# Performance work log

Measured on AMD Instinct MI355X. Metric: run time of the kernel, lower is better.

Reference implementation:

```python
import jax, jax.numpy as jnp
import numpy as np

K = 3
KK = K * K


def conv3x3(x, w, b):
    # x: [B,C,H,W], w: [O,C,3,3]
    y = jax.lax.conv_general_dilated(x, w, (1, 1), ((1, 1), (1, 1)),
                                     dimension_numbers=('NCHW', 'OIHW', 'NCHW'))
    return y + b[None, :, None, None]


def deform_conv(x, offset, w, b):
    # torchvision.ops.deform_conv2d, 3x3, pad=1, stride=1, no mask.
    B, C, H, W = x.shape
    off = offset.reshape(B, KK, 2, H, W)  # per kernel tap: (dy, dx)
    ky = jnp.repeat(jnp.arange(K, dtype=x.dtype) - 1, K)  # [9]
    kx = jnp.tile(jnp.arange(K, dtype=x.dtype) - 1, K)
    py = jnp.arange(H, dtype=x.dtype)[None, None, :, None] + ky[None, :, None, None] + off[:, :, 0]
    px = jnp.arange(W, dtype=x.dtype)[None, None, None, :] + kx[None, :, None, None] + off[:, :, 1]
    y0 = jnp.floor(py)
    x0 = jnp.floor(px)
    wy = (py - y0)[:, None]  # [B,1,9,H,W]
    wx = (px - x0)[:, None]
    y0i = y0.astype(jnp.int32)
    x0i = x0.astype(jnp.int32)
    xf = x.reshape(B, C, H * W)

    def corner(yi, xi):
        valid = ((yi >= 0) & (yi < H) & (xi >= 0) & (xi < W))
        idx = jnp.clip(yi, 0, H - 1) * W + jnp.clip(xi, 0, W - 1)  # [B,9,H,W]
        g = jax.vmap(lambda xb, ib: xb[:, ib.reshape(-1)])(xf, idx)  # [B,C,9*H*W]
        return g.reshape(B, C, KK, H, W) * valid[:, None].astype(x.dtype)

    val = (corner(y0i, x0i) * (1 - wy) * (1 - wx)
           + corner(y0i, x0i + 1) * (1 - wy) * wx
           + corner(y0i + 1, x0i) * wy * (1 - wx)
           + corner(y0i + 1, x0i + 1) * wy * wx)  # [B,C,9,H,W]
    out = jnp.einsum('bckhw,ock->bohw', val, w.reshape(w.shape[0], C, KK))
    return out + b[None, :, None, None]


def se_gate(x, w1, b1, w2, b2):
    # global avg pool -> 1x1 conv -> relu -> 1x1 conv -> sigmoid -> scale
    m = x.mean((2, 3))  # [B,C]
    h = jax.nn.relu(jnp.einsum('bc,rc->br', m, w1) + b1)
    g = jax.nn.sigmoid(jnp.einsum('br,cr->bc', h, w2) + b2)
    return x * g[:, :, None, None]


def resize_bilinear(x, oh, ow):
    # F.interpolate(mode='bilinear', align_corners=False)
    B, C, H, W = x.shape

    def coords(n_in, n_out):
        src = (jnp.arange(n_out, dtype=x.dtype) + 0.5) * (n_in / n_out) - 0.5
        src = jnp.clip(src, 0.0, n_in - 1)
        i0 = jnp.floor(src).astype(jnp.int32)
        i1 = jnp.minimum(i0 + 1, n_in - 1)
        return i0, i1, (src - i0).astype(x.dtype)

    y0, y1, wy = coords(H, oh)
    x = x[:, :, y0, :] * (1 - wy)[None, None, :, None] + x[:, :, y1, :] * wy[None, None, :, None]
    c0, c1, wc = coords(W, ow)
    x = x[:, :, :, c0] * (1 - wc)[None, None, None, :] + x[:, :, :, c1] * wc[None, None, None, :]
    return x


def setup_inputs() -> dict:
    key = jax.random.key(0)
    ks = jax.random.split(key, 12)
    B, C, H, W = 4, 64, 128, 128
    L, O, R = 4, 64, 4  # levels, out_channels, reduction=64//16
    d = {
        'x': jax.random.normal(ks[0], (B, C, H, W), jnp.float32),
        'off_w': jax.random.normal(ks[1], (L, 2 * KK, C, 3, 3), jnp.float32) * 0.01,
        'off_b': jax.random.normal(ks[2], (L, 2 * KK), jnp.float32) * 0.01,
        'dc_w': jax.random.normal(ks[3], (L, O, C, 3, 3), jnp.float32) * 0.05,
        'dc_b': jax.random.normal(ks[4], (L, O), jnp.float32) * 0.05,
        'se_w1': jax.random.normal(ks[5], (L, R, O), jnp.float32) * 0.1,
        'se_b1': jax.random.normal(ks[6], (L, R), jnp.float32) * 0.1,
        'se_w2': jax.random.normal(ks[7], (L, O, R), jnp.float32) * 0.1,
        'se_b2': jax.random.normal(ks[8], (L, O), jnp.float32) * 0.1,
        'fuse_w': jax.random.normal(ks[9], (O, L * O), jnp.float32) * 0.05,
        'fuse_b': jax.random.normal(ks[10], (O,), jnp.float32) * 0.05,
    }
    return d


def reference(x, off_w, off_b, dc_w, dc_b, se_w1, se_b1, se_w2, se_b2, fuse_w, fuse_b):
    B, _, H, W = x.shape
    L = off_w.shape[0]
    cur = x
    feats = []
    for i in range(L):
        if i > 0:
            cur = resize_bilinear(cur, cur.shape[2] // 2, cur.shape[3] // 2)
        off = conv3x3(cur, off_w[i], off_b[i])
        cur = deform_conv(cur, off, dc_w[i], dc_b[i])
        cur = se_gate(cur, se_w1[i], se_b1[i], se_w2[i], se_b2[i])
        feats.append(resize_bilinear(cur, H, W))
    for i in range(L - 2, -1, -1):
        feats[i] = feats[i] + feats[i + 1]
    fused = jnp.concatenate(feats, axis=1)  # [B, L*O, H, W]
    return jnp.einsum('bchw,oc->bohw', fused, fuse_w) + fuse_b[None, :, None, None]
```

## Files before the change

### kernel.cpp

```cpp
#include <hip/hip_runtime.h>
#include <hip/hip_bf16.h>
#include <math.h>


constexpr int Bn = 4;

typedef __attribute__((ext_vector_type(8))) short short8;
typedef __attribute__((ext_vector_type(4))) float f32x4;
typedef __attribute__((ext_vector_type(4))) unsigned uint4v;
typedef __attribute__((ext_vector_type(4))) unsigned short ushort4v;

static __device__ __forceinline__ short f2b(float f){
  union { float f; unsigned u; } v; v.f = f;
  unsigned r = v.u + 0x7fffu + ((v.u >> 16) & 1u);
  return (short)(r >> 16);
}
static __device__ __forceinline__ unsigned f2b2(float x, float y){
  union { __hip_bfloat162 h; unsigned u; } cv;
  cv.h = __float22bfloat162_rn(make_float2(x, y));
  return cv.u;
}
static __device__ __forceinline__ float blo(unsigned u){ return __uint_as_float(u << 16); }
static __device__ __forceinline__ float bhi(unsigned u){ return __uint_as_float(u & 0xffff0000u); }
static __device__ __forceinline__ void pinv(uint4v& x){ asm volatile("" : "+v"(x)); }

constexpr size_t OFF_CUR   = 0;
constexpr size_t OFF_DC    = OFF_CUR  + 4194304;
constexpr size_t OFF_T0    = OFF_DC   + 4194304;
constexpr size_t OFF_T1    = OFF_T0   + 4194304;
constexpr size_t OFF_T2    = OFF_T1   + 1048576;
constexpr size_t OFF_T3    = OFF_T2   + 262144;
constexpr size_t OFF_WSUMT = OFF_T3   + 65536;
constexpr size_t OFF_DCWT  = OFF_WSUMT + 8192;
constexpr size_t OFF_OWT   = OFF_DCWT  + 73728;
constexpr size_t OFF_SUMS  = OFF_OWT   + 36864;

__global__ void prep_k(const float* __restrict__ dc_w, const float* __restrict__ off_w,
                       const float* __restrict__ fuse_w, float* __restrict__ ws){
  int i = blockIdx.x * 256 + threadIdx.x;
  short* dcwT  = (short*)(ws + OFF_DCWT);
  short* owT   = (short*)(ws + OFF_OWT);
  short* wsumT = (short*)(ws + OFF_WSUMT);
  if (i < 147456){
    int oc = i / 576, r = i % 576, k = r >> 6, c = r & 63;
    dcwT[i] = f2b(dc_w[(oc*64 + c)*9 + k]);
  } else if (i < 147456 + 73728){
    int t = i - 147456;
    int lm = t / 576, l = lm >> 5, m = lm & 31, r = t % 576, k = r >> 6, c = r & 63;
    owT[t] = (m < 18) ? f2b(off_w[((l*18 + m)*64 + c)*9 + k]) : (short)0;
  } else if (i < 147456 + 73728 + 16384){
    int t = i - (147456 + 73728);
    int l = t / 4096, r = t % 4096, o = r / 64, c = r % 64;
    float s = 0.f;
    for (int jl = 0; jl <= l; jl++) s += fuse_w[o*256 + jl*64 + c];
    wsumT[t] = f2b(s);
  } else if (i < 147456 + 73728 + 16384 + 65536){
    ws[OFF_SUMS + (i - (147456 + 73728 + 16384))] = 0.f;
  }
}

__global__ __launch_bounds__(256) void cvt_k(const float* __restrict__ x, unsigned* __restrict__ cur){
  __shared__ float t[64][65];
  int tile = blockIdx.x;
  int b = tile >> 8, p0 = (tile & 255) << 6;
  int tx = threadIdx.x & 63, ty = threadIdx.x >> 6;
  #pragma unroll
  for (int c = ty; c < 64; c += 4)
    t[c][tx] = x[(((size_t)(b << 6) + c) << 14) + p0 + tx];
  __syncthreads();
  int u = threadIdx.x & 31, pr = threadIdx.x >> 5;
  #pragma unroll
  for (int i = 0; i < 8; i++){
    int pp = pr + i*8;
    unsigned v = f2b2(t[2*u][pp], t[2*u + 1][pp]);
    cur[((size_t)(b << 14) + p0 + pp)*32 + u] = v;
  }
}

template<int H, int LVL>
__global__ __launch_bounds__(256, 3) void deform8_k(
    const unsigned* __restrict__ cur, const float* __restrict__ ws_all,
    const float* __restrict__ off_bias, const float* __restrict__ dc_bias,
    float* __restrict__ dc, float* __restrict__ sums){
  constexpr int W = H, P = H * W;
  constexpr int PITCHB = 584 * 2;
  constexpr int TPR8 = W/8, TPB8 = P/64;
  __shared__ __align__(16) short valA[16][584];
  __shared__ __align__(16) char  patchS[64*144];
  __shared__ __align__(16) float4 tapW[144];
  __shared__ __align__(8)  unsigned short tapIs[144][4];
  float* offsP = (float*)((char*)&valA[0][0] + 8192);
  const short* owt = (const short*)(ws_all + OFF_OWT) + LVL * 32 * 576;
  const short* dcw = (const short*)(ws_all + OFF_DCWT) + (size_t)LVL * 64 * 576;
  const int tid = threadIdx.x;
  const int wave = tid >> 6, lane = tid & 63;
  const int c0 = lane & 15, quad = lane >> 4, q4 = quad * 4;
  const int b = blockIdx.x / TPB8;
  const int rr = blockIdx.x % TPB8;
  const int hrow8 = (rr / TPR8) * 8, wcol8 = (rr % TPR8) * 8;
  const unsigned* curu = cur + (size_t)b * P * 32;

  uint4v wB[9];
  {
    const short* wrow = owt + ((wave & 1)*16 + c0)*576 + quad*8;
    #pragma unroll
    for (int kb = 0; kb < 9; kb++)
      wB[kb] = *(const uint4v*)&wrow[((wave >> 1)*9 + kb)*32];
    #pragma unroll
    for (int kb = 0; kb < 9; kb++) pinv(wB[kb]);
  }
  const int n = wave*16 + c0;
  uint4v wD[18];
  #pragma unroll
  for (int kb = 0; kb < 18; kb++)
    wD[kb] = *(const uint4v*)&dcw[n*576 + kb*32 + quad*8];
  #pragma unroll
  for (int kb = 0; kb < 18; kb++) pinv(wD[kb]);
  const float bt2 = dc_bias[LVL*64 + n];
  const int tk = tid % 9, tp = tid / 9;
  float oby = 0.f, obx = 0.f;
  if (tid < 144){
    oby = off_bias[LVL*18 + 2*tk];
    obx = off_bias[LVL*18 + 2*tk + 1];
  }
  const int pl = lane >> 3, cq = lane & 7;

  #pragma unroll 1
  for (int t = 0; t < 4; t++){
    const int srow = hrow8 + (t >> 1)*4, scol = wcol8 + (t & 1)*4;
    if (t) __syncthreads();

    #pragma unroll
    for (int i = 0; i < 2; i++){
      int pp = wave*16 + i*8 + pl;
      int R = pp >> 3, C = pp & 7;
      int yy = srow - 2 + R, xx = scol - 2 + C;
      bool v = ((unsigned)yy < (unsigned)H) & ((unsigned)xx < (unsigned)W);
      int idx = v ? (yy*W + xx) : 0;
      uint4 d = *(const uint4*)((const char*)curu + (size_t)idx*128 + cq*16);
      if (!v){ d.x = 0; d.y = 0; d.z = 0; d.w = 0; }
      *(uint4*)(patchS + pp*144 + cq*16) = d;
    }
    __syncthreads();

    {
      const int colw = wave & 1, kh = wave >> 1;
      const char* pb = patchS + (((c0 >> 2) + 1)*8 + (c0 & 3) + 1)*144 + quad*16;
      f32x4 oacc = {0,0,0,0};
      if (kh == 0){
        #pragma unroll
        for (int kb = 0; kb < 9; kb++){
          const int tap = kb >> 1;
          short8 a = *(const short8*)(pb + ((tap/3)*8 + (tap%3))*144 + (kb&1)*64);
          oacc = __builtin_amdgcn_mfma_f32_16x16x32_bf16(a, __builtin_bit_cast(short8, wB[kb]), oacc, 0, 0, 0);
        }
      } else {
        #pragma unroll
        for (int kb = 0; kb < 9; kb++){
          const int kk = 9 + kb, tap = kk >> 1;
          short8 a = *(const short8*)(pb + ((tap/3)*8 + (tap%3))*144 + (kk&1)*64);
          oacc = __builtin_amdgcn_mfma_f32_16x16x32_bf16(a, __builtin_bit_cast(short8, wB[kb]), oacc, 0, 0, 0);
        }
      }
      int comp = colw*16 + c0;
      if (comp < 18){
        #pragma unroll
        for (int r = 0; r < 4; r++) offsP[kh*288 + (q4 + r)*18 + comp] = oacc[r];
      }
    }
    __syncthreads();

    if (tid < 144){
      int p = tp, k = tk;
      int h = srow + (p >> 2), w = scol + (p & 3);
      float oy = offsP[p*18 + 2*k]     + offsP[288 + p*18 + 2*k]     + oby;
      float ox = offsP[p*18 + 2*k + 1] + offsP[288 + p*18 + 2*k + 1] + obx;
      float py = (float)(h + k/3 - 1) + oy;
      float px = (float)(w + k%3 - 1) + ox;
      float y0f = floorf(py), x0f = floorf(px);
      float fy = py - y0f, fx = px - x0f;
      int y0 = (int)y0f, x0 = (int)x0f, y1 = y0 + 1, x1 = x0 + 1;
      bool vy0 = (y0 >= 0) & (y0 < H), vy1 = (y1 >= 0) & (y1 < H);
      bool vx0 = (x0 >= 0) & (x0 < W), vx1 = (x1 >= 0) & (x1 < W);
      int y0c = min(max(y0, 0), H-1), y1c = min(max(y1, 0), H-1);
      int x0c = min(max(x0, 0), W-1), x1c = min(max(x1, 0), W-1);
      float gy = 1.f - fy, gx = 1.f - fx;
      tapW[tid] = make_float4((vy0 & vx0) ? gy*gx : 0.f,
                              (vy0 & vx1) ? gy*fx : 0.f,
                              (vy1 & vx0) ? fy*gx : 0.f,
                              (vy1 & vx1) ? fy*fx : 0.f);
      int ry = y0 - srow + 2, rx = x0 - scol + 2;
      if (((unsigned)ry < 7u) & ((unsigned)rx < 7u)){
        tapIs[tid][0] = (unsigned short)(0x8000u | (ry*8 + rx));
      } else {
        tapIs[tid][0] = (unsigned short)(y0c*W + x0c);
        tapIs[tid][1] = (unsigned short)(y0c*W + x1c);
        tapIs[tid][2] = (unsigned short)(y1c*W + x0c);
        tapIs[tid][3] = (unsigned short)(y1c*W + x1c);
      }
    }
    __syncthreads();

    {
      const char* curc8 = (const char*)curu + c0*8;
      int T = wave*36 + quad;
      int p = wave*4, k = quad;
      #pragma unroll
      for (int i = 0; i < 9; i++){
        float4 wv = tapW[T];
        unsigned short t0 = tapIs[T][0];
        uint2 u0, u1, u2, u3;
        if (t0 & 0x8000u){
          const char* pb2 = patchS + (int)(t0 & 0x7fffu)*144 + c0*8;
          u0 = *(const uint2*)(pb2);
          u1 = *(const uint2*)(pb2 + 144);
          u2 = *(const uint2*)(pb2 + 144*8);
          u3 = *(const uint2*)(pb2 + 144*9);
        } else {
          uint2 tw = *(const uint2*)tapIs[T];
          u0 = *(const uint2*)(curc8 + ((size_t)(tw.x & 0xffffu) << 7));
          u1 = *(const uint2*)(curc8 + ((size_t)(tw.x >> 16)     << 7));
          u2 = *(const uint2*)(curc8 + ((size_t)(tw.y & 0xffffu) << 7));
          u3 = *(const uint2*)(curc8 + ((size_t)(tw.y >> 16)     << 7));
        }
        float a0 = wv.x*blo(u0.x) + wv.y*blo(u1.x) + wv.z*blo(u2.x) + wv.w*blo(u3.x);
        float a1 = wv.x*bhi(u0.x) + wv.y*bhi(u1.x) + wv.z*bhi(u2.x) + wv.w*bhi(u3.x);
        float a2 = wv.x*blo(u0.y) + wv.y*blo(u1.y) + wv.z*blo(u2.y) + wv.w*blo(u3.y);
        float a3 = wv.x*bhi(u0.y) + wv.y*bhi(u1.y) + wv.z*bhi(u2.y) + wv.w*bhi(u3.y);
        uint2 pk; pk.x = f2b2(a0, a1); pk.y = f2b2(a2, a3);
        *(uint2*)((char*)&valA[0][0] + p*PITCHB + k*128 + c0*8) = pk;
        T += 4; k += 4; if (k >= 9){ k -= 9; ++p; }
      }
    }
    __syncthreads();

    f32x4 d0 = {bt2, bt2, bt2, bt2}, d1 = {0,0,0,0};
    #pragma unroll
    for (int kb = 0; kb < 9; kb++){
      short8 a = *(const short8*)&valA[c0][kb*32 + quad*8];
      d0 = __builtin_amdgcn_mfma_f32_16x16x32_bf16(a, __builtin_bit_cast(short8, wD[kb]), d0, 0, 0, 0);
    }
    #pragma unroll
    for (int kb = 9; kb < 18; kb++){
      short8 a = *(const short8*)&valA[c0][kb*32 + quad*8];
      d1 = __builtin_amdgcn_mfma_f32_16x16x32_bf16(a, __builtin_bit_cast(short8, wD[kb]), d1, 0, 0, 0);
    }
    f32x4 acc;
    #pragma unroll
    for (int r = 0; r < 4; r++) acc[r] = d0[r] + d1[r];
    float* dcb = dc + ((size_t)b*P + (size_t)(srow + quad)*W + scol)*64;
    #pragma unroll
    for (int r = 0; r < 4; r++) dcb[r*64 + n] = acc[r];
    float s = acc[0] + acc[1] + acc[2] + acc[3];
    s += __shfl_xor(s, 16);
    s += __shfl_xor(s, 32);
    if (quad == 0) atomicAdd(&sums[(LVL*16 + (blockIdx.x & 15))*256 + (b << 6) + n], s);
  }
}

template<int H, int LVL>
__global__ __launch_bounds__(256, 7) void deform_k(
    const unsigned* __restrict__ cur, const float* __restrict__ ws_all,
    const float* __restrict__ off_bias, const float* __restrict__ dc_bias,
    float* __restrict__ dc, float* __restrict__ sums){
  constexpr int W = H, P = H * W;
  constexpr int PITCHB = 584 * 2;
  constexpr int TPR = W/4, TPB = P/16;
  __shared__ __align__(16) short valA[16][584];
  __shared__ __align__(16) float4 tapW[144];
  __shared__ __align__(8)  unsigned short tapIs[144][4];
  short* patch = &valA[0][0];
  float* offsP = (float*)((char*)&valA[0][0] + 8192);
  const short* owt = (const short*)(ws_all + OFF_OWT) + LVL * 32 * 576;
  const short* dcw = (const short*)(ws_all + OFF_DCWT) + (size_t)LVL * 64 * 576;
  const int tid = threadIdx.x;
  const int wave = tid >> 6, lane = tid & 63;
  const int c0 = lane & 15, quad = lane >> 4, q4 = quad * 4;
  const int b = blockIdx.x / TPB;
  const int rr = blockIdx.x % TPB;
  const int hrow = (rr / TPR) * 4, wcol = (rr % TPR) * 4;
  const unsigned* curu = cur + (size_t)b * P * 32;

  {
    #pragma unroll
    for (int i = 0; i < 3; i++){
      if (i < 2 || quad == 0){
        int p36 = wave*9 + i*4 + quad;
        int r6 = p36 / 6, c6 = p36 - r6*6;
        int yy = hrow - 1 + r6, xx = wcol - 1 + c6;
        bool v = ((unsigned)yy < (unsigned)H) & ((unsigned)xx < (unsigned)W);
        int idx = v ? (yy*W + xx) : 0;
        uint2 d = *(const uint2*)(curu + (size_t)idx*32 + c0*2);
        if (!v){ d.x = 0u; d.y = 0u; }
        *(uint2*)(patch + p36*72 + c0*4) = d;
      }
    }
  }
  __syncthreads();

  {
    const int colw = wave & 1, kh = wave >> 1;
    const char* pb = (const char*)patch + ((c0 >> 2) * 6 + (c0 & 3)) * 144 + quad * 16;
    const short* wrow = owt + (colw*16 + c0)*576 + quad*8;
    f32x4 oacc = {0,0,0,0};
    if (kh == 0){
      #pragma unroll
      for (int kb = 0; kb < 9; kb++){
        const int tap = kb >> 1;
        short8 a  = *(const short8*)(pb + ((tap/3)*864 + (tap%3)*144 + (kb&1)*64));
        short8 bf = *(const short8*)&wrow[kb*32];
        oacc = __builtin_amdgcn_mfma_f32_16x16x32_bf16(a, bf, oacc, 0, 0, 0);
      }
    } else {
      #pragma unroll
      for (int kb = 0; kb < 9; kb++){
        const int kk = 9 + kb, tap = kk >> 1;
        short8 a  = *(const short8*)(pb + ((tap/3)*864 + (tap%3)*144 + (kk&1)*64));
        short8 bf = *(const short8*)&wrow[kk*32];
        oacc = __builtin_amdgcn_mfma_f32_16x16x32_bf16(a, bf, oacc, 0, 0, 0);
      }
    }
    int comp = colw*16 + c0;
    if (comp < 18){
      #pragma unroll
      for (int r = 0; r < 4; r++) offsP[kh*288 + (q4 + r)*18 + comp] = oacc[r];
    }
  }
  __syncthreads();

  if (tid < 144){
    int p = tid / 9, k = tid % 9;
    int h = hrow + (p >> 2), w = wcol + (p & 3);
    float oy = offsP[p*18 + 2*k]     + offsP[288 + p*18 + 2*k]     + off_bias[LVL*18 + 2*k];
    float ox = offsP[p*18 + 2*k + 1] + offsP[288 + p*18 + 2*k + 1] + off_bias[LVL*18 + 2*k + 1];
    float py = (float)(h + k/3 - 1) + oy;
    float px = (float)(w + k%3 - 1) + ox;
    float y0f = floorf(py), x0f = floorf(px);
    float fy = py - y0f, fx = px - x0f;
    int y0 = (int)y0f, x0 = (int)x0f, y1 = y0 + 1, x1 = x0 + 1;
    bool vy0 = (y0 >= 0) & (y0 < H), vy1 = (y1 >= 0) & (y1 < H);
    bool vx0 = (x0 >= 0) & (x0 < W), vx1 = (x1 >= 0) & (x1 < W);
    int y0c = min(max(y0, 0), H-1), y1c = min(max(y1, 0), H-1);
    int x0c = min(max(x0, 0), W-1), x1c = min(max(x1, 0), W-1);
    float gy = 1.f - fy, gx = 1.f - fx;
    tapW[tid] = make_float4((vy0 & vx0) ? gy*gx : 0.f,
                            (vy0 & vx1) ? gy*fx : 0.f,
                            (vy1 & vx0) ? fy*gx : 0.f,
                            (vy1 & vx1) ? fy*fx : 0.f);
    ushort4v ti = { (unsigned short)(y0c*W + x0c), (unsigned short)(y0c*W + x1c),
                    (unsigned short)(y1c*W + x0c), (unsigned short)(y1c*W + x1c) };
    *(ushort4v*)tapIs[tid] = ti;
  }
  __syncthreads();

  {
    const char* curc8 = (const char*)curu + c0*8;
    int T = wave*36 + quad;
    int p = T/9, k = T - p*9;
    #pragma unroll
    for (int i = 0; i < 9; i++){
      float4 wv = tapW[T];
      uint2 tw = *(const uint2*)tapIs[T];
      uint2 u0 = *(const uint2*)(curc8 + ((size_t)(tw.x & 0xffffu) << 7));
      uint2 u1 = *(const uint2*)(curc8 + ((size_t)(tw.x >> 16) << 7));
      uint2 u2 = *(const uint2*)(curc8 + ((size_t)(tw.y & 0xffffu) << 7));
      uint2 u3 = *(const uint2*)(curc8 + ((size_t)(tw.y >> 16) << 7));
      float a0 = wv.x*blo(u0.x) + wv.y*blo(u1.x) + wv.z*blo(u2.x) + wv.w*blo(u3.x);
      float a1 = wv.x*bhi(u0.x) + wv.y*bhi(u1.x) + wv.z*bhi(u2.x) + wv.w*bhi(u3.x);
      float a2 = wv.x*blo(u0.y) + wv.y*blo(u1.y) + wv.z*blo(u2.y) + wv.w*blo(u3.y);
      float a3 = wv.x*bhi(u0.y) + wv.y*bhi(u1.y) + wv.z*bhi(u2.y) + wv.w*bhi(u3.y);
      uint2 pk; pk.x = f2b2(a0, a1); pk.y = f2b2(a2, a3);
      *(uint2*)((char*)&valA[0][0] + p*PITCHB + k*128 + c0*8) = pk;
      T += 4; k += 4; if (k >= 9){ k -= 9; ++p; }
    }
  }
  __syncthreads();

  const int n = wave*16 + c0;
  float bt2 = dc_bias[LVL*64 + n];
  f32x4 d0 = {bt2, bt2, bt2, bt2}, d1 = {0,0,0,0};
  #pragma unroll
  for (int kb = 0; kb < 9; kb++){
    short8 a  = *(const short8*)&valA[c0][kb*32 + quad*8];
    short8 bf = *(const short8*)&dcw[n*576 + kb*32 + quad*8];
    d0 = __builtin_amdgcn_mfma_f32_16x16x32_bf16(a, bf, d0, 0, 0, 0);
  }
  #pragma unroll
  for (int kb = 9; kb < 18; kb++){
    short8 a  = *(const short8*)&valA[c0][kb*32 + quad*8];
    short8 bf = *(const short8*)&dcw[n*576 + kb*32 + quad*8];
    d1 = __builtin_amdgcn_mfma_f32_16x16x32_bf16(a, bf, d1, 0, 0, 0);
  }
  f32x4 acc;
  #pragma unroll
  for (int r = 0; r < 4; r++) acc[r] = d0[r] + d1[r];
  float* dcb = dc + ((size_t)b*P + (size_t)(hrow + quad)*W + wcol)*64;
  #pragma unroll
  for (int r = 0; r < 4; r++) dcb[r*64 + n] = acc[r];
  float s = acc[0] + acc[1] + acc[2] + acc[3];
  s += __shfl_xor(s, 16);
  s += __shfl_xor(s, 32);
  if (quad == 0) atomicAdd(&sums[(LVL*16 + (blockIdx.x & 15))*256 + (b << 6) + n], s);
}

template<int W, int LVL>
__global__ __launch_bounds__(256) void fuse_gd_k(
    const float* __restrict__ dcv, const float* __restrict__ sums,
    const float* __restrict__ se_w1, const float* __restrict__ se_b1,
    const float* __restrict__ se_w2, const float* __restrict__ se_b2,
    const float* __restrict__ ws_all, float* __restrict__ tmp, unsigned* __restrict__ curn){
  constexpr int P = W * W;
  constexpr bool POOL = (LVL < 3);
  constexpr float invP = 1.f / (float)P;
  __shared__ __align__(16) float fS[64][68];
  __shared__ __align__(16) float gsh[64];
  const short* wsl = (const short*)(ws_all + OFF_WSUMT) + LVL * 4096;
  const int tid = threadIdx.x, wave = tid >> 6, lane = tid & 63;
  const int c0 = lane & 15, quad = lane >> 4, q4 = quad * 4;
  int b, rp = 0, cs = 0;
  if (POOL){
    constexpr int tilesPerB = P / 64, tilesPerRow = W / 32;
    b = blockIdx.x / tilesPerB;
    int r = blockIdx.x % tilesPerB;
    rp = r / tilesPerRow; cs = r % tilesPerRow;
  } else {
    b = (blockIdx.x * 64) / P;
  }

  {
    int sg = tid >> 6, c = tid & 63;
    float part = 0.f;
    #pragma unroll
    for (int s = 0; s < 4; s++) part += sums[(LVL*16 + sg*4 + s)*256 + (b << 6) + c];
    fS[sg][c] = part;
    __syncthreads();
    if (tid < 64){
      int r = tid & 3, j = tid >> 2;
      float hp = 0.f;
      #pragma unroll
      for (int q = 0; q < 4; q++){
        int cq = j*4 + q;
        float m = (fS[0][cq] + fS[1][cq] + fS[2][cq] + fS[3][cq]) * invP;
        hp += m * se_w1[(LVL*4 + r)*64 + cq];
      }
      hp += __shfl_xor(hp, 4);  hp += __shfl_xor(hp, 8);
      hp += __shfl_xor(hp, 16); hp += __shfl_xor(hp, 32);
      float hr = fmaxf(hp + se_b1[LVL*4 + r], 0.f);
      float a = se_b2[LVL*64 + tid];
      #pragma unroll
      for (int r2 = 0; r2 < 4; r2++)
        a += __shfl(hr, r2) * se_w2[(LVL*64 + tid)*4 + r2];
      gsh[tid] = 1.f / (1.f + expf(-a));
    }
    __syncthreads();
  }

  float4 g4 = *(const float4*)&gsh[c0*4];
  #pragma unroll
  for (int i = 0; i < 4; i++){
    int lp = wave*16 + (lane >> 4) + i*4;
    size_t gpix = POOL ? ((size_t)b*P + (size_t)(2*rp + (lp >> 5))*W + cs*32 + (lp & 31))
                       : ((size_t)blockIdx.x*64 + lp);
    float4 d = *(const float4*)&dcv[gpix*64 + c0*4];
    float4 v = make_float4(d.x*g4.x, d.y*g4.y, d.z*g4.z, d.w*g4.w);
    *(float4*)&fS[lp][c0*4] = v;
  }
  __syncthreads();
  f32x4 acc[4] = {{0,0,0,0},{0,0,0,0},{0,0,0,0},{0,0,0,0}};
  #pragma unroll
  for (int kb = 0; kb < 2; kb++){
    float4 lo = *(const float4*)&fS[wave*16 + c0][kb*32 + quad*8];
    float4 hi = *(const float4*)&fS[wave*16 + c0][kb*32 + quad*8 + 4];
    uint4v ua = {f2b2(lo.x, lo.y), f2b2(lo.z, lo.w), f2b2(hi.x, hi.y), f2b2(hi.z, hi.w)};
    short8 a = __builtin_bit_cast(short8, ua);
    #pragma unroll
    for (int t = 0; t < 4; t++){
      short8 bf = *(const short8*)&wsl[(t*16 + c0)*64 + kb*32 + quad*8];
      acc[t] = __builtin_amdgcn_mfma_f32_16x16x32_bf16(a, bf, acc[t], 0, 0, 0);
    }
  }
  #pragma unroll
  for (int t = 0; t < 4; t++){
    int n = t*16 + c0;
    size_t plane = ((size_t)(b << 6) + n) * P;
    size_t pix = POOL ? ((size_t)(2*rp + (wave >> 1))*W + cs*32 + (wave & 1)*16 + q4)
                      : ((size_t)(blockIdx.x*64) - (size_t)b*P + wave*16 + q4);
    *(f32x4*)&tmp[plane + pix] = acc[t];
  }
  if constexpr (POOL){
    int j = tid >> 4, uu = tid & 15;
    float4 p0 = *(const float4*)&fS[2*j][uu*4];
    float4 p1 = *(const float4*)&fS[2*j + 1][uu*4];
    float4 p2 = *(const float4*)&fS[32 + 2*j][uu*4];
    float4 p3 = *(const float4*)&fS[33 + 2*j][uu*4];
    float4 av = make_float4(0.25f*(p0.x + p1.x + p2.x + p3.x),
                            0.25f*(p0.y + p1.y + p2.y + p3.y),
                            0.25f*(p0.z + p1.z + p2.z + p3.z),
                            0.25f*(p0.w + p1.w + p2.w + p3.w));
    uint2 pv = make_uint2(f2b2(av.x, av.y), f2b2(av.z, av.w));
    *(uint2*)&curn[((size_t)b*(P/4) + (size_t)rp*(W/2) + cs*16 + j)*32 + uu*2] = pv;
  }
}

__global__ void final_k(const float* __restrict__ ws_all, const float* __restrict__ fuse_bias,
                        float* __restrict__ out){
  int i = blockIdx.x * 256 + threadIdx.x;
  int w = i & 127, h = (i >> 7) & 127, o = (i >> 14) & 63, b = i >> 20;
  float acc = fuse_bias[o] + ws_all[OFF_T0 + (((size_t)(b << 6) + o) << 14) + (h << 7) + w];
  const float* tarr[3] = {ws_all + OFF_T1, ws_all + OFF_T2, ws_all + OFF_T3};
  #pragma unroll
  for (int li = 0; li < 3; li++){
    int l = li + 1, Hl = 128 >> l;
    float scale = 1.0f / (float)(1 << l);
    float sy = fminf(fmaxf((h + 0.5f)*scale - 0.5f, 0.f), (float)(Hl - 1));
    float sx = fminf(fmaxf((w + 0.5f)*scale - 0.5f, 0.f), (float)(Hl - 1));
    int y0 = (int)sy, x0 = (int)sx;
    float fy = sy - y0, fx = sx - x0;
    int y1 = min(y0 + 1, Hl - 1), x1 = min(x0 + 1, Hl - 1);
    const float* tb = tarr[li] + (size_t)((b << 6) + o) * Hl * Hl;
    float v00 = tb[y0*Hl + x0], v01 = tb[y0*Hl + x1];
    float v10 = tb[y1*Hl + x0], v11 = tb[y1*Hl + x1];
    acc += (1.f-fy)*((1.f-fx)*v00 + fx*v01) + fy*((1.f-fx)*v10 + fx*v11);
  }
  out[i] = acc;
}

extern "C" void kernel_launch(void* const* d_in, const int* in_sizes, int n_in,
                              void* d_out, int out_size, void* d_ws, size_t ws_size,
                              hipStream_t stream){
  (void)in_sizes; (void)n_in; (void)out_size; (void)ws_size;
  const float* x      = (const float*)d_in[0];
  const float* off_w  = (const float*)d_in[1];
  const float* off_b  = (const float*)d_in[2];
  const float* dc_w   = (const float*)d_in[3];
  const float* dc_b   = (const float*)d_in[4];
  const float* se_w1  = (const float*)d_in[5];
  const float* se_b1  = (const float*)d_in[6];
  const float* se_w2  = (const float*)d_in[7];
  const float* se_b2  = (const float*)d_in[8];
  const float* fuse_w = (const float*)d_in[9];
  const float* fuse_b = (const float*)d_in[10];
  float* out = (float*)d_out;
  float* ws = (float*)d_ws;
  unsigned* cur = (unsigned*)(ws + OFF_CUR);
  float* dc   = ws + OFF_DC;
  float* tmp[4] = {ws + OFF_T0, ws + OFF_T1, ws + OFF_T2, ws + OFF_T3};
  float* sums = ws + OFF_SUMS;

  prep_k<<<(303104 + 255)/256, 256, 0, stream>>>(dc_w, off_w, fuse_w, ws);
  cvt_k<<<1024, 256, 0, stream>>>(x, cur);

  deform8_k<128,0><<<1024, 256, 0, stream>>>(cur, ws, off_b, dc_b, dc, sums);
  fuse_gd_k<128,0><<<1024, 256, 0, stream>>>(dc, sums, se_w1, se_b1, se_w2, se_b2, ws, tmp[0], cur);
  deform_k<64,1><<<1024, 256, 0, stream>>>(cur, ws, off_b, dc_b, dc, sums);
  fuse_gd_k<64,1><<<256, 256, 0, stream>>>(dc, sums, se_w1, se_b1, se_w2, se_b2, ws, tmp[1], cur);
  deform_k<32,2><<<256, 256, 0, stream>>>(cur, ws, off_b, dc_b, dc, sums);
  fuse_gd_k<32,2><<<64, 256, 0, stream>>>(dc, sums, se_w1, se_b1, se_w2, se_b2, ws, tmp[2], cur);
  deform_k<16,3><<<64, 256, 0, stream>>>(cur, ws, off_b, dc_b, dc, sums);
  fuse_gd_k<16,3><<<16, 256, 0, stream>>>(dc, sums, se_w1, se_b1, se_w2, se_b2, ws, tmp[3], nullptr);

  final_k<<<16384, 256, 0, stream>>>(ws, fuse_b, out);
}
```

Measured before the change: 228.5 us.

## Prefetch next patch tile during gather and reload weights per tile to cut registers

Stops holding the offset-conv and deform-conv weight fragments in registers for the whole kernel and instead reloads them from global or L2 memory inside each MFMA loop, freeing many VGPRs. The next sub-tile's input patch load is issued before the bilinear gather and written to shared memory after the deform MFMAs, overlapping global latency with compute. Tap weights and indices are read into register arrays up front. In exchange, each of the four tiles repeats the weight loads, and the prefetch adds live registers during the gather.

```diff
diff --git a/kernel.cpp b/kernel.cpp
--- a/kernel.cpp
+++ b/kernel.cpp
@@ -22,7 +22,6 @@
 }
 static __device__ __forceinline__ float blo(unsigned u){ return __uint_as_float(u << 16); }
 static __device__ __forceinline__ float bhi(unsigned u){ return __uint_as_float(u & 0xffff0000u); }
-static __device__ __forceinline__ void pinv(uint4v& x){ asm volatile("" : "+v"(x)); }
 
 constexpr size_t OFF_CUR   = 0;
 constexpr size_t OFF_DC    = OFF_CUR  + 4194304;
@@ -99,23 +98,7 @@
   const int rr = blockIdx.x % TPB8;
   const int hrow8 = (rr / TPR8) * 8, wcol8 = (rr % TPR8) * 8;
   const unsigned* curu = cur + (size_t)b * P * 32;
-
-  uint4v wB[9];
-  {
-    const short* wrow = owt + ((wave & 1)*16 + c0)*576 + quad*8;
-    #pragma unroll
-    for (int kb = 0; kb < 9; kb++)
-      wB[kb] = *(const uint4v*)&wrow[((wave >> 1)*9 + kb)*32];
-    #pragma unroll
-    for (int kb = 0; kb < 9; kb++) pinv(wB[kb]);
-  }
   const int n = wave*16 + c0;
-  uint4v wD[18];
-  #pragma unroll
-  for (int kb = 0; kb < 18; kb++)
-    wD[kb] = *(const uint4v*)&dcw[n*576 + kb*32 + quad*8];
-  #pragma unroll
-  for (int kb = 0; kb < 18; kb++) pinv(wD[kb]);
   const float bt2 = dc_bias[LVL*64 + n];
   const int tk = tid % 9, tp = tid / 9;
   float oby = 0.f, obx = 0.f;
@@ -125,41 +108,54 @@
   }
   const int pl = lane >> 3, cq = lane & 7;
 
+  uint4 hA0, hA1; bool vA0 = false, vA1 = false;
+  auto issueA = [&](int srow, int scol){
+    int pp0 = wave*16 + pl;
+    int yy0 = srow - 2 + (pp0 >> 3), xx0 = scol - 2 + (pp0 & 7);
+    vA0 = ((unsigned)yy0 < (unsigned)H) & ((unsigned)xx0 < (unsigned)W);
+    hA0 = *(const uint4*)((const char*)curu + (size_t)(vA0 ? (yy0*W + xx0) : 0)*128 + cq*16);
+    int pp1 = pp0 + 8;
+    int yy1 = srow - 2 + (pp1 >> 3), xx1 = scol - 2 + (pp1 & 7);
+    vA1 = ((unsigned)yy1 < (unsigned)H) & ((unsigned)xx1 < (unsigned)W);
+    hA1 = *(const uint4*)((const char*)curu + (size_t)(vA1 ? (yy1*W + xx1) : 0)*128 + cq*16);
+  };
+  auto storeA = [&](){
+    const uint4 z = make_uint4(0, 0, 0, 0);
+    int pp0 = wave*16 + pl;
+    uint4 d0 = vA0 ? hA0 : z;
+    uint4 d1 = vA1 ? hA1 : z;
+    *(uint4*)(patchS + pp0*144 + cq*16) = d0;
+    *(uint4*)(patchS + (pp0 + 8)*144 + cq*16) = d1;
+  };
+
+  issueA(hrow8, wcol8);
+  storeA();
+
   #pragma unroll 1
   for (int t = 0; t < 4; t++){
     const int srow = hrow8 + (t >> 1)*4, scol = wcol8 + (t & 1)*4;
-    if (t) __syncthreads();
-
-    #pragma unroll
-    for (int i = 0; i < 2; i++){
-      int pp = wave*16 + i*8 + pl;
-      int R = pp >> 3, C = pp & 7;
-      int yy = srow - 2 + R, xx = scol - 2 + C;
-      bool v = ((unsigned)yy < (unsigned)H) & ((unsigned)xx < (unsigned)W);
-      int idx = v ? (yy*W + xx) : 0;
-      uint4 d = *(const uint4*)((const char*)curu + (size_t)idx*128 + cq*16);
-      if (!v){ d.x = 0; d.y = 0; d.z = 0; d.w = 0; }
-      *(uint4*)(patchS + pp*144 + cq*16) = d;
-    }
     __syncthreads();
 
     {
       const int colw = wave & 1, kh = wave >> 1;
       const char* pb = patchS + (((c0 >> 2) + 1)*8 + (c0 & 3) + 1)*144 + quad*16;
+      const short* wrow = owt + (colw*16 + c0)*576 + quad*8;
       f32x4 oacc = {0,0,0,0};
       if (kh == 0){
         #pragma unroll
         for (int kb = 0; kb < 9; kb++){
           const int tap = kb >> 1;
-          short8 a = *(const short8*)(pb + ((tap/3)*8 + (tap%3))*144 + (kb&1)*64);
-          oacc = __builtin_amdgcn_mfma_f32_16x16x32_bf16(a, __builtin_bit_cast(short8, wB[kb]), oacc, 0, 0, 0);
+          short8 a  = *(const short8*)(pb + ((tap/3)*8 + (tap%3))*144 + (kb&1)*64);
+          short8 bf = *(const short8*)&wrow[kb*32];
+          oacc = __builtin_amdgcn_mfma_f32_16x16x32_bf16(a, bf, oacc, 0, 0, 0);
         }
       } else {
         #pragma unroll
         for (int kb = 0; kb < 9; kb++){
           const int kk = 9 + kb, tap = kk >> 1;
-          short8 a = *(const short8*)(pb + ((tap/3)*8 + (tap%3))*144 + (kk&1)*64);
-          oacc = __builtin_amdgcn_mfma_f32_16x16x32_bf16(a, __builtin_bit_cast(short8, wB[kb]), oacc, 0, 0, 0);
+          short8 a  = *(const short8*)(pb + ((tap/3)*8 + (tap%3))*144 + (kk&1)*64);
+          short8 bf = *(const short8*)&wrow[kk*32];
+          oacc = __builtin_amdgcn_mfma_f32_16x16x32_bf16(a, bf, oacc, 0, 0, 0);
         }
       }
       int comp = colw*16 + c0;
@@ -201,23 +197,32 @@
     }
     __syncthreads();
 
+    if (t < 3){
+      const int nt = t + 1;
+      issueA(hrow8 + (nt >> 1)*4, wcol8 + (nt & 1)*4);
+    }
     {
       const char* curc8 = (const char*)curu + c0*8;
-      int T = wave*36 + quad;
+      const int T0 = wave*36 + quad;
+      float4 wvr[9]; uint2 twr[9];
+      #pragma unroll
+      for (int i = 0; i < 9; i++){
+        wvr[i] = tapW[T0 + 4*i];
+        twr[i] = *(const uint2*)tapIs[T0 + 4*i];
+      }
       int p = wave*4, k = quad;
       #pragma unroll
       for (int i = 0; i < 9; i++){
-        float4 wv = tapW[T];
-        unsigned short t0 = tapIs[T][0];
+        float4 wv = wvr[i];
+        uint2 tw = twr[i];
         uint2 u0, u1, u2, u3;
-        if (t0 & 0x8000u){
-          const char* pb2 = patchS + (int)(t0 & 0x7fffu)*144 + c0*8;
+        if (tw.x & 0x8000u){
+          const char* pb2 = patchS + (int)(tw.x & 0x7fffu)*144 + c0*8;
           u0 = *(const uint2*)(pb2);
           u1 = *(const uint2*)(pb2 + 144);
           u2 = *(const uint2*)(pb2 + 144*8);
           u3 = *(const uint2*)(pb2 + 144*9);
         } else {
-          uint2 tw = *(const uint2*)tapIs[T];
           u0 = *(const uint2*)(curc8 + ((size_t)(tw.x & 0xffffu) << 7));
           u1 = *(const uint2*)(curc8 + ((size_t)(tw.x >> 16)     << 7));
           u2 = *(const uint2*)(curc8 + ((size_t)(tw.y & 0xffffu) << 7));
@@ -229,7 +234,7 @@
         float a3 = wv.x*bhi(u0.y) + wv.y*bhi(u1.y) + wv.z*bhi(u2.y) + wv.w*bhi(u3.y);
         uint2 pk; pk.x = f2b2(a0, a1); pk.y = f2b2(a2, a3);
         *(uint2*)((char*)&valA[0][0] + p*PITCHB + k*128 + c0*8) = pk;
-        T += 4; k += 4; if (k >= 9){ k -= 9; ++p; }
+        k += 4; if (k >= 9){ k -= 9; ++p; }
       }
     }
     __syncthreads();
@@ -237,14 +242,17 @@
     f32x4 d0 = {bt2, bt2, bt2, bt2}, d1 = {0,0,0,0};
     #pragma unroll
     for (int kb = 0; kb < 9; kb++){
-      short8 a = *(const short8*)&valA[c0][kb*32 + quad*8];
-      d0 = __builtin_amdgcn_mfma_f32_16x16x32_bf16(a, __builtin_bit_cast(short8, wD[kb]), d0, 0, 0, 0);
+      short8 a  = *(const short8*)&valA[c0][kb*32 + quad*8];
+      short8 bf = *(const short8*)&dcw[n*576 + kb*32 + quad*8];
+      d0 = __builtin_amdgcn_mfma_f32_16x16x32_bf16(a, bf, d0, 0, 0, 0);
     }
     #pragma unroll
     for (int kb = 9; kb < 18; kb++){
-      short8 a = *(const short8*)&valA[c0][kb*32 + quad*8];
-      d1 = __builtin_amdgcn_mfma_f32_16x16x32_bf16(a, __builtin_bit_cast(short8, wD[kb]), d1, 0, 0, 0);
-    }
+      short8 a  = *(const short8*)&valA[c0][kb*32 + quad*8];
+      short8 bf = *(const short8*)&dcw[n*576 + kb*32 + quad*8];
+      d1 = __builtin_amdgcn_mfma_f32_16x16x32_bf16(a, bf, d1, 0, 0, 0);
+    }
+    if (t < 3) storeA();
     f32x4 acc;
     #pragma unroll
     for (int r = 0; r < 4; r++) acc[r] = d0[r] + d1[r];
```

Result: slower. 253.5 us (+11.0%).
